# Kernel optimization log

Measured on AMD Instinct MI355X. Metric: run time of the kernel, lower is better.

Reference implementation:

```python
import jax, jax.numpy as jnp
import numpy as np

N = 20000   # nodes
E = 320000  # edges
T = 12      # sequence_length
H = 64      # hidden_dim
CIN = 16    # input_dim_per_step
L = 3       # num_st_layers
BN_EPS = 1e-5


def setup_inputs() -> dict:
    key = jax.random.key(0)
    ks = jax.random.split(key, 30)
    s = 0.05
    rn = lambda k, shp: jax.random.normal(k, shp, jnp.float32) * s
    inp = {
        "x": jax.random.normal(ks[0], (N, T * CIN), jnp.float32),
        "edge_index": jax.random.randint(ks[1], (2, E), 0, N, jnp.int32),
        # embedding
        "We": rn(ks[2], (CIN, H)), "be": rn(ks[3], (H,)),
        # stacked per-layer params for the 3 ST layers
        "gcn_W": rn(ks[4], (L, H, H)), "gcn_b": rn(ks[5], (L, H)),
        "conv_w": rn(ks[6], (L, H, H, 3)), "conv_b": rn(ks[7], (L, H)),
        "bn_g": jnp.ones((L, H), jnp.float32), "bn_b": rn(ks[8], (L, H)),
        "bn_m": rn(ks[9], (L, H)),
        "bn_v": jax.random.uniform(ks[10], (L, H), jnp.float32, 0.5, 1.5),
        # temporal attention MLP (H -> H//2 -> 1)
        "ta_w1": rn(ks[11], (H, H // 2)), "ta_b1": rn(ks[12], (H // 2,)),
        "ta_w2": rn(ks[13], (H // 2, 1)), "ta_b2": rn(ks[14], (1,)),
        # feature attention MLP (T -> T//2 -> 1)
        "fa_w1": rn(ks[15], (T, T // 2)), "fa_b1": rn(ks[16], (T // 2,)),
        "fa_w2": rn(ks[17], (T // 2, 1)), "fa_b2": rn(ks[18], (1,)),
        # output MLP (H -> H//2 -> 1)
        "ow1": rn(ks[19], (H, H // 2)), "ob1": rn(ks[20], (H // 2,)),
        "ow2": rn(ks[21], (H // 2, 1)), "ob2": rn(ks[22], (1,)),
    }
    return inp


def reference(x, edge_index, We, be, gcn_W, gcn_b, conv_w, conv_b,
              bn_g, bn_b, bn_m, bn_v, ta_w1, ta_b1, ta_w2, ta_b2,
              fa_w1, fa_b1, fa_w2, fa_b2, ow1, ob1, ow2, ob2):
    n = x.shape[0]
    # --- GCN normalization with self-loops (PyG gcn_norm) ---
    loops = jnp.arange(n, dtype=edge_index.dtype)
    src = jnp.concatenate([edge_index[0], loops])
    dst = jnp.concatenate([edge_index[1], loops])
    deg = jax.ops.segment_sum(jnp.ones_like(src, jnp.float32), dst, num_segments=n)
    dinv = 1.0 / jnp.sqrt(deg)  # deg >= 1 thanks to self-loops
    coef = dinv[src] * dinv[dst]  # [E+N]

    # --- per-timestep embedding (vectorized over t) ---
    xr = x.reshape(n, T, CIN)
    emb = jax.nn.relu(jnp.einsum('ntc,ch->nth', xr, We) + be)  # [N,T,H]
    x_st = emb.reshape(n, T * H)

    # --- ST layers (replicating original row-major .view layout mixing) ---
    for i in range(L):
        xi = x_st.reshape(n, H, T)  # [N,C,T]
        # GCNConv per timestep, batched over t: linear then normalized aggregate
        h = jnp.einsum('nct,cd->ndt', xi, gcn_W[i])          # [N,H,T]
        msg = coef[:, None, None] * h[src]                   # [E+N,H,T]
        agg = jax.ops.segment_sum(msg, dst, num_segments=n) + gcn_b[i][None, :, None]
        # temporal conv (kernel 3, pad 1) over T
        tmp = jax.lax.conv_general_dilated(
            agg, conv_w[i], (1,), [(1, 1)],
            dimension_numbers=('NCH', 'OIH', 'NCH')) + conv_b[i][None, :, None]
        # BatchNorm1d (eval mode: running stats)
        normed = (tmp - bn_m[i][None, :, None]) / jnp.sqrt(bn_v[i][None, :, None] + BN_EPS)
        normed = normed * bn_g[i][None, :, None] + bn_b[i][None, :, None]
        # residual is Identity (in_channels == out_channels)
        x_st = jax.nn.relu(normed + xi).reshape(n, H * T)

    # --- dual attention pooling ---
    xa = x_st.reshape(n, T, H)
    tw = (jnp.einsum('ntm,mk->ntk', jax.nn.relu(jnp.einsum('nth,hm->ntm', xa, ta_w1) + ta_b1), ta_w2) + ta_b2)[..., 0]
    tw = jax.nn.softmax(tw, axis=1)                          # [N,T]
    xt = (xa * tw[..., None]).transpose(0, 2, 1)             # [N,H,T]
    fw = (jnp.einsum('nhm,mk->nhk', jax.nn.relu(jnp.einsum('nht,tm->nhm', xt, fa_w1) + fa_b1), fa_w2) + fa_b2)[..., 0]
    fw = jax.nn.softmax(fw, axis=1)                          # [N,H]
    x_final = jnp.sum(xt * fw[..., None], axis=2)            # [N,H]

    # --- output MLP (dropout is identity in eval) ---
    out = jax.nn.relu(x_final @ ow1 + ob1) @ ow2 + ob2       # [N,1]
    return out
```

## Files before the change

### kernel.cpp

```cpp
#include <hip/hip_runtime.h>
#include <cstddef>
#include <cstdint>

#define T_ 12
#define H_ 64
#define CIN_ 16
#define F_ 768
#define PAD_ROW 772
#define BN_EPS 1e-5f
#define ECAP 80
#define RPITCH 88

typedef float v2f __attribute__((ext_vector_type(2)));
typedef short s8v __attribute__((ext_vector_type(8)));
typedef float f4v __attribute__((ext_vector_type(4)));

__device__ __forceinline__ unsigned short f2bf(float f) {
    unsigned u = __float_as_uint(f);
    unsigned r = (u + 0x7FFFu + ((u >> 16) & 1u)) >> 16;
    return (unsigned short)r;
}
__device__ __forceinline__ float bf2f(unsigned short h) {
    return __uint_as_float(((unsigned)h) << 16);
}
__device__ __forceinline__ v2f bf2x2(unsigned u) {
    v2f r;
    r.x = __uint_as_float(u << 16);
    r.y = __uint_as_float(u & 0xFFFF0000u);
    return r;
}
__device__ __forceinline__ v2f pkfma(v2f a, v2f b, v2f c) {
    return __builtin_elementwise_fma(a, b, c);
}


__global__ void k_init(int* __restrict__ cnt, int* __restrict__ cursor, int n) {
    int i = blockIdx.x * 256 + threadIdx.x;
    if (i < n) { cnt[i] = 0; cursor[i] = 0; }
}

__global__ void k_count(const int* __restrict__ dstv, int* __restrict__ cnt, int e) {
    int i = blockIdx.x * 256 + threadIdx.x;
    if (i < e) atomicAdd(&cnt[dstv[i]], 1);
}

__global__ __launch_bounds__(1024) void k_scan1(const int* __restrict__ cnt,
                                                int* __restrict__ row_local,
                                                int* __restrict__ bsum, int n) {
    __shared__ int sd[1024];
    int tid = threadIdx.x;
    int i = blockIdx.x * 1024 + tid;
    int v = (i < n) ? cnt[i] : 0;
    sd[tid] = v;
    __syncthreads();
    for (int off = 1; off < 1024; off <<= 1) {
        int t = (tid >= off) ? sd[tid - off] : 0;
        __syncthreads();
        sd[tid] += t;
        __syncthreads();
    }
    if (i < n) row_local[i] = sd[tid] - v;
    if (tid == 1023) bsum[blockIdx.x] = sd[1023];
}

__global__ __launch_bounds__(64) void k_scan2(const int* __restrict__ bsum,
                                              int* __restrict__ boff, int nb,
                                              int* __restrict__ row_start, int n) {
    int lane = threadIdx.x;
    int orig = (lane < nb) ? bsum[lane] : 0;
    int v = orig;
    for (int off = 1; off < 64; off <<= 1) {
        int t = __shfl_up(v, off);
        if (lane >= off) v += t;
    }
    if (lane < nb) boff[lane] = v - orig;
    if (lane == 63) row_start[n] = v;
}

__global__ __launch_bounds__(1024) void k_scan3(const int* __restrict__ row_local,
                                                const int* __restrict__ boff,
                                                const int* __restrict__ cnt,
                                                int* __restrict__ row_start,
                                                float* __restrict__ dinv, int n) {
    int i = blockIdx.x * 1024 + threadIdx.x;
    if (i < n) {
        row_start[i] = row_local[i] + boff[blockIdx.x];
        dinv[i] = rsqrtf((float)(cnt[i] + 1));
    }
}

__global__ void k_scatter(const int* __restrict__ srcv, const int* __restrict__ dstv,
                          const int* __restrict__ row_start, int* __restrict__ cursor,
                          const float* __restrict__ dinv, int* __restrict__ csr_src,
                          float* __restrict__ csr_coef, int e) {
    int i = blockIdx.x * 256 + threadIdx.x;
    if (i < e) {
        int d = dstv[i], s = srcv[i];
        int pos = atomicAdd(&cursor[d], 1);
        int idx = row_start[d] + pos;
        csr_src[idx]  = s;
        csr_coef[idx] = dinv[s] * dinv[d];
    }
}


__global__ __launch_bounds__(256) void k_wprep(const float* __restrict__ gcn_W,
                                               const float* __restrict__ gcn_b,
                                               const float* __restrict__ conv_w,
                                               float* __restrict__ wkp,
                                               float* __restrict__ bkp) {
    int b = blockIdx.x;
    int l = b / 12, k = (b / 4) % 3, cq = b & 3;
    const float* Wg = gcn_W + (size_t)l * 4096;
    const float* cw = conv_w + (size_t)l * 12288;
    int tid = threadIdx.x;
#pragma unroll
    for (int j = 0; j < 4; j++) {
        int idx = j * 256 + tid;
        int c = cq * 16 + (idx >> 6);
        int o = idx & 63;
        float acc = 0.f;
        for (int d = 0; d < 64; d++)
            acc += Wg[c * 64 + d] * cw[(size_t)(o * 64 + d) * 3 + k];
        wkp[(((size_t)l * 3 + k) * 64 + c) * 64 + o] = acc;
    }
    if (cq == 0 && tid < 64) {
        int o = tid;
        const float* gb = gcn_b + (size_t)l * 64;
        float acc = 0.f;
        for (int d = 0; d < 64; d++)
            acc += gb[d] * cw[(size_t)(o * 64 + d) * 3 + k];
        bkp[((size_t)l * 3 + k) * 64 + o] = acc;
    }
}

__global__ __launch_bounds__(64) void k_wpack(const float* __restrict__ wkp,
                                              unsigned short* __restrict__ wkA) {
    int b = blockIdx.x;
    int l = b / 24, rem = b % 24;
    int mt = rem / 6, ks = rem % 6;
    int lane = threadIdx.x;
    int o = mt * 16 + (lane & 15);
    int kbase = ks * 32 + (lane >> 4) * 8;
#pragma unroll
    for (int j = 0; j < 8; j++) {
        int k = kbase + j;
        int kk = k >> 6, c = k & 63;
        float v = wkp[(((size_t)l * 3 + kk) * 64 + c) * 64 + o];
        wkA[((((size_t)l * 24) + mt * 6 + ks) * 64 + lane) * 8 + j] = f2bf(v);
    }
}


__global__ __launch_bounds__(256) void k_embed(const float* __restrict__ x,
                                               const float* __restrict__ We,
                                               const float* __restrict__ be,
                                               unsigned short* __restrict__ xbf,
                                               int nT) {
    __shared__ float sW[CIN_ * H_];
    __shared__ float sb[H_];
    for (int i = threadIdx.x; i < CIN_ * H_; i += 256) sW[i] = We[i];
    if (threadIdx.x < H_) sb[threadIdx.x] = be[threadIdx.x];
    __syncthreads();
    int h4  = threadIdx.x & 15;
    int ntl = threadIdx.x >> 4;
    int nt  = blockIdx.x * 16 + ntl;
    if (nt >= nT) return;
    const float4* xp = (const float4*)(x + (size_t)nt * CIN_);
    float4 xv4[4];
    xv4[0] = xp[0]; xv4[1] = xp[1]; xv4[2] = xp[2]; xv4[3] = xp[3];
    const float* xs = (const float*)xv4;
    float acc[4];
#pragma unroll
    for (int j = 0; j < 4; j++) acc[j] = sb[h4 * 4 + j];
#pragma unroll
    for (int c = 0; c < CIN_; c++) {
        float4 w = *(const float4*)&sW[c * H_ + h4 * 4];
        float xc = xs[c];
        acc[0] += xc * w.x; acc[1] += xc * w.y; acc[2] += xc * w.z; acc[3] += xc * w.w;
    }
    ushort4 h;
    h.x = f2bf(fmaxf(acc[0], 0.f)); h.y = f2bf(fmaxf(acc[1], 0.f));
    h.z = f2bf(fmaxf(acc[2], 0.f)); h.w = f2bf(fmaxf(acc[3], 0.f));
    *(ushort4*)&xbf[(size_t)nt * H_ + h4 * 4] = h;
}


#define BPK(aL, aH, c2, u) { \
    aL = pkfma(bf2x2((u).x), c2, aL); \
    aH = pkfma(bf2x2((u).y), c2, aH); }

__global__ __launch_bounds__(256, 7) void k_layer(
        const unsigned short* __restrict__ xin,
        unsigned short* __restrict__ xout,
        const int* __restrict__ row_start, const int* __restrict__ csr_src,
        const float* __restrict__ csr_coef, const float* __restrict__ dinv,
        const unsigned short* __restrict__ wkA,
        const float* __restrict__ bkp,
        const float* __restrict__ cb,
        const float* __restrict__ bng, const float* __restrict__ bnb,
        const float* __restrict__ bnm, const float* __restrict__ bnv,
        int n) {
    __shared__ __align__(16) unsigned short sxb[8 * 14 * RPITCH];
    __shared__ int se[4 * ECAP * 2];
    int tid = threadIdx.x;
    int n0 = blockIdx.x * 8;
    int wave = tid >> 6, lane = tid & 63;
    int wbase = wave * (ECAP * 2);

    for (int i = tid; i < 8 * 2 * RPITCH; i += 256) {
        int s = i / (2 * RPITCH);
        int r = i - s * (2 * RPITCH);
        int row = (r < RPITCH) ? 0 : 13;
        int c = (r < RPITCH) ? r : r - RPITCH;
        sxb[s * 14 * RPITCH + row * RPITCH + c] = 0;
    }

    int begs[2], cnts[2], stgs[2], epos[2];
    {
        int pos = 0;
#pragma unroll
        for (int si = 0; si < 2; si++) {
            int nn = n0 + wave * 2 + si; if (nn >= n) nn = n - 1;
            int beg = row_start[nn], end = row_start[nn + 1];
            int cnt = end - beg;
            int stg = min(cnt, ECAP - pos);
            for (int i = lane; i < stg; i += 64) {
                se[wbase + (pos + i) * 2]     = csr_src[beg + i];
                se[wbase + (pos + i) * 2 + 1] = __float_as_int(csr_coef[beg + i]);
            }
            begs[si] = beg; cnts[si] = cnt; stgs[si] = stg; epos[si] = pos;
            pos += stg;
        }
    }

    {
        int i0 = 3 * lane;
#pragma unroll
        for (int si = 0; si < 2; si++) {
            int s = wave * 2 + si;
            int nn = n0 + s; if (nn >= n) nn = n - 1;
            float dn = dinv[nn];
            float cs = dn * dn;
            v2f cs2 = {cs, cs};
            const uint2* xp = (const uint2*)(xin + (size_t)nn * F_);
            uint2 u0 = xp[i0], u1 = xp[i0 + 1], u2 = xp[i0 + 2];
            v2f a0 = bf2x2(u0.x) * cs2, a1 = bf2x2(u0.y) * cs2;
            v2f a2 = bf2x2(u1.x) * cs2, a3 = bf2x2(u1.y) * cs2;
            v2f a4 = bf2x2(u2.x) * cs2, a5 = bf2x2(u2.y) * cs2;
            int cnt = stgs[si];
            int base = wbase + epos[si] * 2;
            int e = 0;
            for (; e + 3 < cnt; e += 4) {
                int2 p0 = *(const int2*)&se[base + e * 2];
                int2 p1 = *(const int2*)&se[base + e * 2 + 2];
                int2 p2 = *(const int2*)&se[base + e * 2 + 4];
                int2 p3 = *(const int2*)&se[base + e * 2 + 6];
                const uint2* pA = (const uint2*)(xin + (size_t)p0.x * F_);
                const uint2* pB = (const uint2*)(xin + (size_t)p1.x * F_);
                const uint2* pC = (const uint2*)(xin + (size_t)p2.x * F_);
                const uint2* pD = (const uint2*)(xin + (size_t)p3.x * F_);
                uint2 uA0 = pA[i0], uA1 = pA[i0 + 1], uA2 = pA[i0 + 2];
                uint2 uB0 = pB[i0], uB1 = pB[i0 + 1], uB2 = pB[i0 + 2];
                uint2 uC0 = pC[i0], uC1 = pC[i0 + 1], uC2 = pC[i0 + 2];
                uint2 uD0 = pD[i0], uD1 = pD[i0 + 1], uD2 = pD[i0 + 2];
                float cA = __int_as_float(p0.y), cB = __int_as_float(p1.y);
                float cC = __int_as_float(p2.y), cD = __int_as_float(p3.y);
                v2f cA2 = {cA, cA}, cB2 = {cB, cB}, cC2 = {cC, cC}, cD2 = {cD, cD};
                BPK(a0, a1, cA2, uA0) BPK(a2, a3, cA2, uA1) BPK(a4, a5, cA2, uA2)
                BPK(a0, a1, cB2, uB0) BPK(a2, a3, cB2, uB1) BPK(a4, a5, cB2, uB2)
                BPK(a0, a1, cC2, uC0) BPK(a2, a3, cC2, uC1) BPK(a4, a5, cC2, uC2)
                BPK(a0, a1, cD2, uD0) BPK(a2, a3, cD2, uD1) BPK(a4, a5, cD2, uD2)
            }
            for (; e < cnt; e++) {
                int2 p0 = *(const int2*)&se[base + e * 2];
                const uint2* pA = (const uint2*)(xin + (size_t)p0.x * F_);
                uint2 uA0 = pA[i0], uA1 = pA[i0 + 1], uA2 = pA[i0 + 2];
                float cA = __int_as_float(p0.y);
                v2f cA2 = {cA, cA};
                BPK(a0, a1, cA2, uA0) BPK(a2, a3, cA2, uA1) BPK(a4, a5, cA2, uA2)
            }
            for (int g = begs[si] + stgs[si]; g < begs[si] + cnts[si]; g++) {
                int srcI = csr_src[g];
                float cf = csr_coef[g];
                const uint2* pA = (const uint2*)(xin + (size_t)srcI * F_);
                uint2 uA0 = pA[i0], uA1 = pA[i0 + 1], uA2 = pA[i0 + 2];
                v2f cf2 = {cf, cf};
                BPK(a0, a1, cf2, uA0) BPK(a2, a3, cf2, uA1) BPK(a4, a5, cf2, uA2)
            }
            unsigned short* wp = &sxb[s * 14 * RPITCH + RPITCH + lane];
            float vals[12] = {a0.x, a0.y, a1.x, a1.y, a2.x, a2.y,
                              a3.x, a3.y, a4.x, a4.y, a5.x, a5.y};
#pragma unroll
            for (int t = 0; t < 12; t++) wp[t * RPITCH] = f2bf(vals[t]);
        }
    }
    __syncthreads();

    int mt = wave;
    int q = lane >> 4;
    int l15 = lane & 15;
    s8v afr[6];
    const s8v* Ap = (const s8v*)wkA;
#pragma unroll
    for (int ks = 0; ks < 6; ks++) afr[ks] = Ap[(mt * 6 + ks) * 64 + lane];
    int obase = mt * 16 + q * 4;
    float scl[4], shf[4], ball[4], bk0a[4], bk2a[4];
#pragma unroll
    for (int r = 0; r < 4; r++) {
        int o = obase + r;
        float sc = bng[o] * rsqrtf(bnv[o] + BN_EPS);
        scl[r] = sc;
        shf[r] = bnb[o] - bnm[o] * sc;
        float b0 = bkp[o], b1 = bkp[64 + o], b2 = bkp[128 + o];
        ball[r] = cb[o] + b0 + b1 + b2;
        bk0a[r] = b0; bk2a[r] = b2;
    }
    f4v accv[6];
#pragma unroll
    for (int nt = 0; nt < 6; nt++) {
        int nidx = nt * 16 + l15;
        int s = nidx / 12, t = nidx - 12 * s;
        const s8v* bp = (const s8v*)&sxb[s * 14 * RPITCH + t * RPITCH + q * 8];
        f4v acc = {0.f, 0.f, 0.f, 0.f};
        acc = __builtin_amdgcn_mfma_f32_16x16x32_bf16(afr[0], bp[0],  acc, 0, 0, 0);
        acc = __builtin_amdgcn_mfma_f32_16x16x32_bf16(afr[1], bp[4],  acc, 0, 0, 0);
        acc = __builtin_amdgcn_mfma_f32_16x16x32_bf16(afr[2], bp[11], acc, 0, 0, 0);
        acc = __builtin_amdgcn_mfma_f32_16x16x32_bf16(afr[3], bp[15], acc, 0, 0, 0);
        acc = __builtin_amdgcn_mfma_f32_16x16x32_bf16(afr[4], bp[22], acc, 0, 0, 0);
        acc = __builtin_amdgcn_mfma_f32_16x16x32_bf16(afr[5], bp[26], acc, 0, 0, 0);
        accv[nt] = acc;
    }
    __syncthreads();

#pragma unroll
    for (int nt = 0; nt < 6; nt++) {
        int nidx = nt * 16 + l15;
        int s = nidx / 12, t = nidx - 12 * s;
        unsigned short* dp = &sxb[s * F_ + t];
#pragma unroll
        for (int r = 0; r < 4; r++) {
            float bias = ball[r];
            if (t == 0)  bias -= bk0a[r];
            if (t == 11) bias -= bk2a[r];
            float v = (accv[nt][r] + bias) * scl[r] + shf[r];
            dp[(obase + r) * 12] = f2bf(v);
        }
    }
    __syncthreads();

#pragma unroll
    for (int cidx = 0; cidx < 3; cidx++) {
        int c = cidx * 256 + tid;
        int s = c / 96, off = c - s * 96;
        int nn = n0 + s;
        if (nn >= n) continue;
        uint4 dv = *(const uint4*)&sxb[s * F_ + off * 8];
        const uint4* rrow = (const uint4*)(xin + (size_t)nn * F_);
        uint4 rv = rrow[off];
        uint4 ov;
        unsigned* dvp = (unsigned*)&dv;
        unsigned* rvp = (unsigned*)&rv;
        unsigned* ovp = (unsigned*)&ov;
#pragma unroll
        for (int w = 0; w < 4; w++) {
            v2f d2 = bf2x2(dvp[w]);
            v2f r2 = bf2x2(rvp[w]);
            float lo = fmaxf(d2.x + r2.x, 0.f);
            float hi = fmaxf(d2.y + r2.y, 0.f);
            ovp[w] = (unsigned)f2bf(lo) | ((unsigned)f2bf(hi) << 16);
        }
        *(uint4*)(xout + (size_t)nn * F_ + off * 8) = ov;
    }
}


__global__ __launch_bounds__(128) void k_attn(const unsigned short* __restrict__ xst,
        const float* __restrict__ taw1, const float* __restrict__ tab1,
        const float* __restrict__ taw2, const float* __restrict__ tab2,
        const float* __restrict__ faw1, const float* __restrict__ fab1,
        const float* __restrict__ faw2, const float* __restrict__ fab2,
        const float* __restrict__ ow1, const float* __restrict__ ob1,
        const float* __restrict__ ow2, const float* __restrict__ ob2,
        float* __restrict__ out, int n) {
    __shared__ float sT[8 * PAD_ROW];
    __shared__ float s_tab1[32], s_taw2[32], s_ob1[32], s_ow2[32];
    __shared__ float s_faw1[72], s_fab1[8], s_faw2[8];
    __shared__ float s_tw[8 * 12];
    __shared__ float s_xf[8 * 65];
    int tid = threadIdx.x;
    int n0 = blockIdx.x * 8;
    if (tid < 32) {
        s_tab1[tid] = tab1[tid]; s_taw2[tid] = taw2[tid];
        s_ob1[tid] = ob1[tid];   s_ow2[tid] = ow2[tid];
    }
    if (tid < 72) s_faw1[tid] = faw1[tid];
    if (tid < 6) { s_fab1[tid] = fab1[tid]; s_faw2[tid] = faw2[tid]; }
    float tb2 = tab2[0], fb2 = fab2[0], o_b2 = ob2[0];
    for (int i = tid * 4; i < 8 * F_; i += 512) {
        int s = i / F_, j = i - s * F_;
        int nn = n0 + s; if (nn >= n) nn = n - 1;
        ushort4 v = *(const ushort4*)&xst[(size_t)nn * F_ + j];
        int t = j >> 6, hh = j & 63;
        float* dst = &sT[s * PAD_ROW + hh * 12 + t];
        dst[0]  = bf2f(v.x);
        dst[12] = bf2f(v.y);
        dst[24] = bf2f(v.z);
        dst[36] = bf2f(v.w);
    }
    __syncthreads();

    int s = tid >> 4, m2 = tid & 15;
    {
        v2f a[12];
        v2f bb = *((const v2f*)s_tab1 + m2);
#pragma unroll
        for (int t = 0; t < 12; t++) a[t] = bb;
        const float* xr = &sT[s * PAD_ROW];
        const v2f* twp = (const v2f*)taw1 + m2;
        for (int hh = 0; hh < 64; hh++) {
            float4 q0 = *(const float4*)&xr[hh * 12];
            float4 q1 = *(const float4*)&xr[hh * 12 + 4];
            float4 q2 = *(const float4*)&xr[hh * 12 + 8];
            float xv[12] = {q0.x, q0.y, q0.z, q0.w, q1.x, q1.y, q1.z, q1.w, q2.x, q2.y, q2.z, q2.w};
            v2f wv = twp[hh * 16];
#pragma unroll
            for (int t = 0; t < 12; t++)
                a[t] = pkfma(wv, (v2f){xv[t], xv[t]}, a[t]);
        }
        float w20 = s_taw2[2 * m2], w21 = s_taw2[2 * m2 + 1];
#pragma unroll
        for (int t = 0; t < 12; t++) {
            float p = fmaxf(a[t].x, 0.f) * w20 + fmaxf(a[t].y, 0.f) * w21;
            p += __shfl_xor(p, 1); p += __shfl_xor(p, 2);
            p += __shfl_xor(p, 4); p += __shfl_xor(p, 8);
            if (m2 == 0) s_tw[s * 12 + t] = p + tb2;
        }
    }
    __syncthreads();

    int wave = tid >> 6, lane = tid & 63;
    for (int q = 0; q < 4; q++) {
        int ss = wave * 4 + q;
        float tw[12];
#pragma unroll
        for (int t = 0; t < 12; t++) tw[t] = s_tw[ss * 12 + t];
        float mx = tw[0];
#pragma unroll
        for (int t = 1; t < 12; t++) mx = fmaxf(mx, tw[t]);
        float sum = 0.f;
#pragma unroll
        for (int t = 0; t < 12; t++) { tw[t] = __expf(tw[t] - mx); sum += tw[t]; }
        float inv = 1.f / sum;
        const float* xr = &sT[ss * PAD_ROW + lane * 12];
        float4 q0 = *(const float4*)(xr);
        float4 q1 = *(const float4*)(xr + 4);
        float4 q2 = *(const float4*)(xr + 8);
        float xv[12] = {q0.x, q0.y, q0.z, q0.w, q1.x, q1.y, q1.z, q1.w, q2.x, q2.y, q2.z, q2.w};
        float xt[12];
#pragma unroll
        for (int t = 0; t < 12; t++) xt[t] = xv[t] * tw[t] * inv;
        float lf = fb2;
#pragma unroll
        for (int mm = 0; mm < 6; mm++) {
            float v = s_fab1[mm];
#pragma unroll
            for (int t = 0; t < 12; t++) v += xt[t] * s_faw1[t * 6 + mm];
            lf += fmaxf(v, 0.f) * s_faw2[mm];
        }
        float m2v = lf;
#pragma unroll
        for (int off = 32; off >= 1; off >>= 1) m2v = fmaxf(m2v, __shfl_xor(m2v, off));
        float e = __expf(lf - m2v);
        float se = e;
#pragma unroll
        for (int off = 32; off >= 1; off >>= 1) se += __shfl_xor(se, off);
        float fwv = e / se;
        float xs = 0.f;
#pragma unroll
        for (int t = 0; t < 12; t++) xs += xt[t];
        s_xf[ss * 65 + lane] = fwv * xs;
    }
    __syncthreads();

    {
        float v0 = s_ob1[2 * m2], v1 = s_ob1[2 * m2 + 1];
        const float* xfp = &s_xf[s * 65];
        for (int hh = 0; hh < 64; hh++) {
            float xv = xfp[hh];
            float2 wv = *(const float2*)&ow1[hh * 32 + 2 * m2];
            v0 += xv * wv.x;
            v1 += xv * wv.y;
        }
        float p = fmaxf(v0, 0.f) * s_ow2[2 * m2] + fmaxf(v1, 0.f) * s_ow2[2 * m2 + 1];
        p += __shfl_xor(p, 1); p += __shfl_xor(p, 2);
        p += __shfl_xor(p, 4); p += __shfl_xor(p, 8);
        if (m2 == 0 && n0 + s < n) out[n0 + s] = p + o_b2;
    }
}


extern "C" void kernel_launch(void* const* d_in, const int* in_sizes, int n_in,
                              void* d_out, int out_size, void* d_ws, size_t ws_size,
                              hipStream_t stream) {
    const float* x      = (const float*)d_in[0];
    const int*   ei     = (const int*)d_in[1];
    const float* We     = (const float*)d_in[2];
    const float* be     = (const float*)d_in[3];
    const float* gcn_W  = (const float*)d_in[4];
    const float* gcn_b  = (const float*)d_in[5];
    const float* conv_w = (const float*)d_in[6];
    const float* conv_b = (const float*)d_in[7];
    const float* bn_g   = (const float*)d_in[8];
    const float* bn_b   = (const float*)d_in[9];
    const float* bn_m   = (const float*)d_in[10];
    const float* bn_v   = (const float*)d_in[11];
    const float* ta_w1  = (const float*)d_in[12];
    const float* ta_b1  = (const float*)d_in[13];
    const float* ta_w2  = (const float*)d_in[14];
    const float* ta_b2  = (const float*)d_in[15];
    const float* fa_w1  = (const float*)d_in[16];
    const float* fa_b1  = (const float*)d_in[17];
    const float* fa_w2  = (const float*)d_in[18];
    const float* fa_b2  = (const float*)d_in[19];
    const float* ow1    = (const float*)d_in[20];
    const float* ob1    = (const float*)d_in[21];
    const float* ow2    = (const float*)d_in[22];
    const float* ob2    = (const float*)d_in[23];

    int n = in_sizes[0] / (T_ * CIN_);
    int e = in_sizes[1] / 2;
    const int* srcv = ei;
    const int* dstv = ei + e;

    char* p = (char*)d_ws;
    auto take = [&](size_t bytes) -> void* {
        void* r = (void*)p;
        p += (bytes + 255) & ~(size_t)255;
        return r;
    };
    int*   cnt       = (int*)take((size_t)n * 4);
    int*   cursor    = (int*)take((size_t)n * 4);
    int*   row_start = (int*)take(((size_t)n + 1) * 4);
    int*   row_local = (int*)take((size_t)n * 4);
    int*   bsum      = (int*)take(1024 * 4);
    int*   boff      = (int*)take(1024 * 4);
    float* dinv      = (float*)take((size_t)n * 4);
    int*   csr_src   = (int*)take((size_t)e * 4);
    float* csr_coef  = (float*)take((size_t)e * 4);
    float* wkp       = (float*)take((size_t)3 * 3 * 64 * 64 * 4);
    float* bkp       = (float*)take((size_t)3 * 3 * 64 * 4);
    unsigned short* wkA = (unsigned short*)take((size_t)3 * 24 * 64 * 8 * 2);
    unsigned short* xabf = (unsigned short*)take((size_t)n * F_ * 2);
    unsigned short* xbbf = (unsigned short*)take((size_t)n * F_ * 2);

    int nb_n = (n + 255) / 256;
    int nb_e = (e + 255) / 256;
    int nb_s = (n + 1023) / 1024;
    int nb8  = (n + 7) / 8;

    k_wprep<<<36, 256, 0, stream>>>(gcn_W, gcn_b, conv_w, wkp, bkp);
    k_wpack<<<72, 64, 0, stream>>>(wkp, wkA);
    k_init<<<nb_n, 256, 0, stream>>>(cnt, cursor, n);
    k_count<<<nb_e, 256, 0, stream>>>(dstv, cnt, e);
    k_scan1<<<nb_s, 1024, 0, stream>>>(cnt, row_local, bsum, n);
    k_scan2<<<1, 64, 0, stream>>>(bsum, boff, nb_s, row_start, n);
    k_scan3<<<nb_s, 1024, 0, stream>>>(row_local, boff, cnt, row_start, dinv, n);
    k_scatter<<<nb_e, 256, 0, stream>>>(srcv, dstv, row_start, cursor, dinv,
                                        csr_src, csr_coef, e);

    int nT = n * T_;
    k_embed<<<(nT + 15) / 16, 256, 0, stream>>>(x, We, be, xabf, nT);

    const unsigned short* curbf = xabf;
    for (int i = 0; i < 3; i++) {
        unsigned short* nxtbf = (curbf == xabf) ? xbbf : xabf;
        k_layer<<<nb8, 256, 0, stream>>>(curbf, nxtbf,
                                         row_start, csr_src, csr_coef, dinv,
                                         wkA + (size_t)i * 24 * 64 * 8,
                                         bkp + (size_t)i * 3 * 64,
                                         conv_b + (size_t)i * H_,
                                         bn_g + (size_t)i * H_, bn_b + (size_t)i * H_,
                                         bn_m + (size_t)i * H_, bn_v + (size_t)i * H_,
                                         n);
        curbf = nxtbf;
    }

    k_attn<<<nb8, 128, 0, stream>>>(curbf, ta_w1, ta_b1, ta_w2, ta_b2,
                                    fa_w1, fa_b1, fa_w2, fa_b2,
                                    ow1, ob1, ow2, ob2, (float*)d_out, n);
}
```

Baseline: 482.4 us.

## Merge graph preprocessing, embedding, and weight prep into fewer launches

Replaces the three-kernel multi-block scan with a single-block scan that computes row starts and dinv directly. The CSR scatter, embedding, weight fold/pack and bias fold now run as one heterogeneous launch, and the zeroing kernel becomes a memset. This removes about seven kernel launches and the serial gaps between them. In exchange the scan runs on one workgroup with strided per-thread chunks, which gives uncoalesced reads, and the weight packing now recomputes the fold per packed element.

Measured after the change: 533.9 us. 1.11x slower.

```diff
diff --git a/kernel.cpp b/kernel.cpp
--- a/kernel.cpp
+++ b/kernel.cpp
@@ -34,24 +34,22 @@
 }
 
 
-__global__ void k_init(int* __restrict__ cnt, int* __restrict__ cursor, int n) {
-    int i = blockIdx.x * 256 + threadIdx.x;
-    if (i < n) { cnt[i] = 0; cursor[i] = 0; }
-}
-
 __global__ void k_count(const int* __restrict__ dstv, int* __restrict__ cnt, int e) {
     int i = blockIdx.x * 256 + threadIdx.x;
     if (i < e) atomicAdd(&cnt[dstv[i]], 1);
 }
 
-__global__ __launch_bounds__(1024) void k_scan1(const int* __restrict__ cnt,
-                                                int* __restrict__ row_local,
-                                                int* __restrict__ bsum, int n) {
+__global__ __launch_bounds__(1024) void k_scanall(const int* __restrict__ cnt,
+                                                  int* __restrict__ row_start,
+                                                  float* __restrict__ dinv, int n) {
     __shared__ int sd[1024];
     int tid = threadIdx.x;
-    int i = blockIdx.x * 1024 + tid;
-    int v = (i < n) ? cnt[i] : 0;
-    sd[tid] = v;
+    int chunk = (n + 1023) >> 10;
+    int beg = tid * chunk;
+    int end = min(beg + chunk, n);
+    int sum = 0;
+    for (int i = beg; i < end; i++) sum += cnt[i];
+    sd[tid] = sum;
     __syncthreads();
     for (int off = 1; off < 1024; off <<= 1) {
         int t = (tid >= off) ? sd[tid - off] : 0;
@@ -59,130 +57,105 @@
         sd[tid] += t;
         __syncthreads();
     }
-    if (i < n) row_local[i] = sd[tid] - v;
-    if (tid == 1023) bsum[blockIdx.x] = sd[1023];
-}
-
-__global__ __launch_bounds__(64) void k_scan2(const int* __restrict__ bsum,
-                                              int* __restrict__ boff, int nb,
-                                              int* __restrict__ row_start, int n) {
-    int lane = threadIdx.x;
-    int orig = (lane < nb) ? bsum[lane] : 0;
-    int v = orig;
-    for (int off = 1; off < 64; off <<= 1) {
-        int t = __shfl_up(v, off);
-        if (lane >= off) v += t;
-    }
-    if (lane < nb) boff[lane] = v - orig;
-    if (lane == 63) row_start[n] = v;
-}
-
-__global__ __launch_bounds__(1024) void k_scan3(const int* __restrict__ row_local,
-                                                const int* __restrict__ boff,
-                                                const int* __restrict__ cnt,
-                                                int* __restrict__ row_start,
-                                                float* __restrict__ dinv, int n) {
-    int i = blockIdx.x * 1024 + threadIdx.x;
-    if (i < n) {
-        row_start[i] = row_local[i] + boff[blockIdx.x];
-        dinv[i] = rsqrtf((float)(cnt[i] + 1));
-    }
-}
-
-__global__ void k_scatter(const int* __restrict__ srcv, const int* __restrict__ dstv,
-                          const int* __restrict__ row_start, int* __restrict__ cursor,
-                          const float* __restrict__ dinv, int* __restrict__ csr_src,
-                          float* __restrict__ csr_coef, int e) {
-    int i = blockIdx.x * 256 + threadIdx.x;
-    if (i < e) {
-        int d = dstv[i], s = srcv[i];
-        int pos = atomicAdd(&cursor[d], 1);
-        int idx = row_start[d] + pos;
-        csr_src[idx]  = s;
-        csr_coef[idx] = dinv[s] * dinv[d];
-    }
-}
-
-
-__global__ __launch_bounds__(256) void k_wprep(const float* __restrict__ gcn_W,
-                                               const float* __restrict__ gcn_b,
-                                               const float* __restrict__ conv_w,
-                                               float* __restrict__ wkp,
-                                               float* __restrict__ bkp) {
-    int b = blockIdx.x;
-    int l = b / 12, k = (b / 4) % 3, cq = b & 3;
-    const float* Wg = gcn_W + (size_t)l * 4096;
-    const float* cw = conv_w + (size_t)l * 12288;
-    int tid = threadIdx.x;
-#pragma unroll
-    for (int j = 0; j < 4; j++) {
-        int idx = j * 256 + tid;
-        int c = cq * 16 + (idx >> 6);
-        int o = idx & 63;
-        float acc = 0.f;
-        for (int d = 0; d < 64; d++)
-            acc += Wg[c * 64 + d] * cw[(size_t)(o * 64 + d) * 3 + k];
-        wkp[(((size_t)l * 3 + k) * 64 + c) * 64 + o] = acc;
-    }
-    if (cq == 0 && tid < 64) {
-        int o = tid;
-        const float* gb = gcn_b + (size_t)l * 64;
-        float acc = 0.f;
-        for (int d = 0; d < 64; d++)
-            acc += gb[d] * cw[(size_t)(o * 64 + d) * 3 + k];
-        bkp[((size_t)l * 3 + k) * 64 + o] = acc;
-    }
-}
-
-__global__ __launch_bounds__(64) void k_wpack(const float* __restrict__ wkp,
-                                              unsigned short* __restrict__ wkA) {
-    int b = blockIdx.x;
-    int l = b / 24, rem = b % 24;
-    int mt = rem / 6, ks = rem % 6;
-    int lane = threadIdx.x;
-    int o = mt * 16 + (lane & 15);
-    int kbase = ks * 32 + (lane >> 4) * 8;
-#pragma unroll
-    for (int j = 0; j < 8; j++) {
-        int k = kbase + j;
-        int kk = k >> 6, c = k & 63;
-        float v = wkp[(((size_t)l * 3 + kk) * 64 + c) * 64 + o];
-        wkA[((((size_t)l * 24) + mt * 6 + ks) * 64 + lane) * 8 + j] = f2bf(v);
-    }
-}
-
-
-__global__ __launch_bounds__(256) void k_embed(const float* __restrict__ x,
-                                               const float* __restrict__ We,
-                                               const float* __restrict__ be,
-                                               unsigned short* __restrict__ xbf,
-                                               int nT) {
+    int run = (tid > 0) ? sd[tid - 1] : 0;
+    for (int i = beg; i < end; i++) {
+        int c = cnt[i];
+        row_start[i] = run;
+        run += c;
+        dinv[i] = rsqrtf((float)(c + 1));
+    }
+    if (tid == 1023) row_start[n] = sd[1023];
+}
+
+
+__global__ __launch_bounds__(256) void k_misc(
+        const int* __restrict__ srcv, const int* __restrict__ dstv,
+        const int* __restrict__ row_start, int* __restrict__ cursor,
+        const float* __restrict__ dinv, int* __restrict__ csr_src,
+        float* __restrict__ csr_coef, int e,
+        const float* __restrict__ x, const float* __restrict__ We,
+        const float* __restrict__ be, unsigned short* __restrict__ xbf, int nT,
+        const float* __restrict__ gcn_W, const float* __restrict__ gcn_b,
+        const float* __restrict__ conv_w,
+        unsigned short* __restrict__ wkA, float* __restrict__ bkp,
+        int nbE, int nbM) {
     __shared__ float sW[CIN_ * H_];
     __shared__ float sb[H_];
-    for (int i = threadIdx.x; i < CIN_ * H_; i += 256) sW[i] = We[i];
-    if (threadIdx.x < H_) sb[threadIdx.x] = be[threadIdx.x];
-    __syncthreads();
-    int h4  = threadIdx.x & 15;
-    int ntl = threadIdx.x >> 4;
-    int nt  = blockIdx.x * 16 + ntl;
-    if (nt >= nT) return;
-    const float4* xp = (const float4*)(x + (size_t)nt * CIN_);
-    float4 xv4[4];
-    xv4[0] = xp[0]; xv4[1] = xp[1]; xv4[2] = xp[2]; xv4[3] = xp[3];
-    const float* xs = (const float*)xv4;
-    float acc[4];
-#pragma unroll
-    for (int j = 0; j < 4; j++) acc[j] = sb[h4 * 4 + j];
-#pragma unroll
-    for (int c = 0; c < CIN_; c++) {
-        float4 w = *(const float4*)&sW[c * H_ + h4 * 4];
-        float xc = xs[c];
-        acc[0] += xc * w.x; acc[1] += xc * w.y; acc[2] += xc * w.z; acc[3] += xc * w.w;
-    }
-    ushort4 h;
-    h.x = f2bf(fmaxf(acc[0], 0.f)); h.y = f2bf(fmaxf(acc[1], 0.f));
-    h.z = f2bf(fmaxf(acc[2], 0.f)); h.w = f2bf(fmaxf(acc[3], 0.f));
-    *(ushort4*)&xbf[(size_t)nt * H_ + h4 * 4] = h;
+    int b = blockIdx.x;
+    int tid = threadIdx.x;
+
+    if (b < nbE) {
+        int i = b * 256 + tid;
+        if (i < e) {
+            int d = dstv[i], s = srcv[i];
+            int pos = atomicAdd(&cursor[d], 1);
+            int idx = row_start[d] + pos;
+            csr_src[idx]  = s;
+            csr_coef[idx] = dinv[s] * dinv[d];
+        }
+        return;
+    }
+    if (b < nbE + nbM) {
+        for (int i = tid; i < CIN_ * H_; i += 256) sW[i] = We[i];
+        if (tid < H_) sb[tid] = be[tid];
+        __syncthreads();
+        int h4  = tid & 15;
+        int ntl = tid >> 4;
+        int nt  = (b - nbE) * 16 + ntl;
+        if (nt >= nT) return;
+        const float4* xp = (const float4*)(x + (size_t)nt * CIN_);
+        float4 xv4[4];
+        xv4[0] = xp[0]; xv4[1] = xp[1]; xv4[2] = xp[2]; xv4[3] = xp[3];
+        const float* xs = (const float*)xv4;
+        float acc[4];
+#pragma unroll
+        for (int j = 0; j < 4; j++) acc[j] = sb[h4 * 4 + j];
+#pragma unroll
+        for (int c = 0; c < CIN_; c++) {
+            float4 w = *(const float4*)&sW[c * H_ + h4 * 4];
+            float xc = xs[c];
+            acc[0] += xc * w.x; acc[1] += xc * w.y;
+            acc[2] += xc * w.z; acc[3] += xc * w.w;
+        }
+        ushort4 h;
+        h.x = f2bf(fmaxf(acc[0], 0.f)); h.y = f2bf(fmaxf(acc[1], 0.f));
+        h.z = f2bf(fmaxf(acc[2], 0.f)); h.w = f2bf(fmaxf(acc[3], 0.f));
+        *(ushort4*)&xbf[(size_t)nt * H_ + h4 * 4] = h;
+        return;
+    }
+    if (b < nbE + nbM + 18) {
+        int wave = tid >> 6, lane = tid & 63;
+        int job = (b - nbE - nbM) * 4 + wave;
+        int l = job / 24, rem = job % 24;
+        int mt = rem / 6, ks = rem % 6;
+        const float* Wg = gcn_W + (size_t)l * 4096;
+        const float* cw = conv_w + (size_t)l * 12288;
+        int o = mt * 16 + (lane & 15);
+        int kbase = ks * 32 + (lane >> 4) * 8;
+#pragma unroll
+        for (int j = 0; j < 8; j++) {
+            int k = kbase + j;
+            int kk = k >> 6, c = k & 63;
+            float acc = 0.f;
+            for (int d = 0; d < 64; d++)
+                acc += Wg[c * 64 + d] * cw[(size_t)(o * 64 + d) * 3 + kk];
+            wkA[((((size_t)l * 24) + mt * 6 + ks) * 64 + lane) * 8 + j] = f2bf(acc);
+        }
+        return;
+    }
+    {
+        int l = b - nbE - nbM - 18;
+        if (tid < 192) {
+            int kk = tid / 64, o = tid & 63;
+            const float* gb = gcn_b + (size_t)l * 64;
+            const float* cw = conv_w + (size_t)l * 12288;
+            float acc = 0.f;
+            for (int d = 0; d < 64; d++)
+                acc += gb[d] * cw[(size_t)(o * 64 + d) * 3 + kk];
+            bkp[((size_t)l * 3 + kk) * 64 + o] = acc;
+        }
+        return;
+    }
 }
 
 
@@ -539,38 +512,30 @@
         p += (bytes + 255) & ~(size_t)255;
         return r;
     };
+    size_t nA = ((size_t)n * 4 + 255) & ~(size_t)255;
     int*   cnt       = (int*)take((size_t)n * 4);
     int*   cursor    = (int*)take((size_t)n * 4);
     int*   row_start = (int*)take(((size_t)n + 1) * 4);
-    int*   row_local = (int*)take((size_t)n * 4);
-    int*   bsum      = (int*)take(1024 * 4);
-    int*   boff      = (int*)take(1024 * 4);
     float* dinv      = (float*)take((size_t)n * 4);
     int*   csr_src   = (int*)take((size_t)e * 4);
     float* csr_coef  = (float*)take((size_t)e * 4);
-    float* wkp       = (float*)take((size_t)3 * 3 * 64 * 64 * 4);
     float* bkp       = (float*)take((size_t)3 * 3 * 64 * 4);
     unsigned short* wkA = (unsigned short*)take((size_t)3 * 24 * 64 * 8 * 2);
     unsigned short* xabf = (unsigned short*)take((size_t)n * F_ * 2);
     unsigned short* xbbf = (unsigned short*)take((size_t)n * F_ * 2);
 
-    int nb_n = (n + 255) / 256;
     int nb_e = (e + 255) / 256;
-    int nb_s = (n + 1023) / 1024;
+    int nT   = n * T_;
+    int nbM  = (nT + 15) / 16;
     int nb8  = (n + 7) / 8;
 
-    k_wprep<<<36, 256, 0, stream>>>(gcn_W, gcn_b, conv_w, wkp, bkp);
-    k_wpack<<<72, 64, 0, stream>>>(wkp, wkA);
-    k_init<<<nb_n, 256, 0, stream>>>(cnt, cursor, n);
+    hipMemsetAsync(cnt, 0, nA * 2, stream);
     k_count<<<nb_e, 256, 0, stream>>>(dstv, cnt, e);
-    k_scan1<<<nb_s, 1024, 0, stream>>>(cnt, row_local, bsum, n);
-    k_scan2<<<1, 64, 0, stream>>>(bsum, boff, nb_s, row_start, n);
-    k_scan3<<<nb_s, 1024, 0, stream>>>(row_local, boff, cnt, row_start, dinv, n);
-    k_scatter<<<nb_e, 256, 0, stream>>>(srcv, dstv, row_start, cursor, dinv,
-                                        csr_src, csr_coef, e);
-
-    int nT = n * T_;
-    k_embed<<<(nT + 15) / 16, 256, 0, stream>>>(x, We, be, xabf, nT);
+    k_scanall<<<1, 1024, 0, stream>>>(cnt, row_start, dinv, n);
+    k_misc<<<nb_e + nbM + 18 + 3, 256, 0, stream>>>(
+        srcv, dstv, row_start, cursor, dinv, csr_src, csr_coef, e,
+        x, We, be, xabf, nT,
+        gcn_W, gcn_b, conv_w, wkA, bkp, nb_e, nbM);
 
     const unsigned short* curbf = xabf;
     for (int i = 0; i < 3; i++) {
```
